# Performance work log

Hardware: AMD Instinct MI355X
Metric: run time of the kernel (lower is better)

## Reference

```python
import jax, jax.numpy as jnp
import numpy as np

N = 100000      # nodes
E = 1600000     # edges
F_IN = 64       # num_node_features
R = 8           # num_relations
G = 256         # graphs in batch
H, C = 4, 32    # GAT heads, per-head channels
NEG_SLOPE_ATT = 0.2    # GATConv attention leaky relu
NEG_SLOPE = 0.01       # F.leaky_relu default


def setup_inputs() -> dict:
    key = jax.random.key(0)
    ks = jax.random.split(key, 12)
    init = lambda k, shape, fan: (jax.random.normal(k, shape, jnp.float32) / np.sqrt(fan).astype(np.float32))
    x = jax.random.normal(ks[0], (N, F_IN), jnp.float32)
    edge_index = jax.random.randint(ks[1], (2, E), 0, N)
    edge_type = jax.random.randint(ks[2], (E,), 0, R)
    batch = (jnp.arange(N) * G) // N  # sorted graph ids, every segment non-empty
    return dict(
        x=x, edge_index=edge_index, edge_type=edge_type, batch=batch,
        gat_w=init(ks[3], (F_IN, H * C), F_IN),
        gat_att_src=init(ks[4], (H, C), C),
        gat_att_dst=init(ks[5], (H, C), C),
        gat_bias=jnp.zeros((H * C,), jnp.float32),
        dense1_w=init(ks[6], (H * C, 16), H * C),
        dense1_b=jnp.zeros((16,), jnp.float32),
        rw1=init(ks[7], (R, F_IN, 32), F_IN),
        root1=init(ks[8], (F_IN, 32), F_IN),
        rb1=jnp.zeros((32,), jnp.float32),
        rw2=init(ks[9], (R, 32, 16), 32),
        root2=init(ks[10], (32, 16), 32),
        rb2=jnp.zeros((16,), jnp.float32),
        dense_w=init(ks[11], (32, 1), 32),
        dense_b=jnp.zeros((1,), jnp.float32),
    )


def _gat(x, src, dst, w, att_src, att_dst, bias):
    h = (x @ w).reshape(N, H, C)                       # [N,H,C]
    a_src = jnp.sum(h * att_src, axis=-1)              # [N,H]
    a_dst = jnp.sum(h * att_dst, axis=-1)              # [N,H]
    e = jax.nn.leaky_relu(a_src[src] + a_dst[dst], NEG_SLOPE_ATT)  # [E,H]
    # segment softmax over incoming edges of each dst node
    m = jax.ops.segment_max(e, dst, num_segments=N)    # [N,H]
    p = jnp.exp(e - m[dst])
    s = jax.ops.segment_sum(p, dst, num_segments=N)    # [N,H]
    alpha = p / s[dst]
    msg = h[src] * alpha[:, :, None]                   # [E,H,C]
    out = jax.ops.segment_sum(msg, dst, num_segments=N)
    return out.reshape(N, H * C) + bias


def _rgcn(x, src, dst, edge_type, w, root, bias):
    # per-relation transform of all nodes, then edge gather (PyG RGCNConv, aggr='mean')
    xw = jnp.einsum('ni,rio->rno', x, w)               # [R,N,out]
    msg = xw[edge_type, src]                           # [E,out]
    comb = dst * R + edge_type                         # mean is per (dst, relation)
    cnt = jax.ops.segment_sum(jnp.ones((E,), x.dtype), comb, num_segments=N * R)
    agg = jax.ops.segment_sum(msg / cnt[comb][:, None], dst, num_segments=N)
    return agg + x @ root + bias


def reference(x, edge_index, edge_type, batch, gat_w, gat_att_src, gat_att_dst,
              gat_bias, dense1_w, dense1_b, rw1, root1, rb1, rw2, root2, rb2,
              dense_w, dense_b):
    src, dst = edge_index[0], edge_index[1]
    # GAT branch (dropout treated as identity / eval mode)
    h = _gat(x, src, dst, gat_w, gat_att_src, gat_att_dst, gat_bias)
    h = jax.nn.leaky_relu(h, NEG_SLOPE)
    h = jax.nn.leaky_relu(h @ dense1_w + dense1_b, NEG_SLOPE)
    gmax = jax.ops.segment_max(h, batch, num_segments=G)          # [G,16]
    # RGCN branch
    z = jax.nn.relu(_rgcn(x, src, dst, edge_type, rw1, root1, rb1))
    z = jax.nn.relu(_rgcn(z, src, dst, edge_type, rw2, root2, rb2))
    nodes_per_graph = jax.ops.segment_sum(jnp.ones((N,), x.dtype), batch, num_segments=G)
    gmean = jax.ops.segment_sum(z, batch, num_segments=G) / nodes_per_graph[:, None]
    # fuse
    zc = jnp.concatenate([gmax, gmean], axis=1)                   # [G,32]
    return zc @ dense_w + dense_b                                  # [G,1]
```

## Files before the change

kernel.cpp:

```cpp
#include <hip/hip_runtime.h>
#include <hip/hip_bf16.h>

typedef __hip_bfloat16 bf16;
typedef unsigned short u16;

#define N_NODES 100000
#define N_EDGES 1600000
#define F_IN 64
#define N_REL 8
#define N_GRAPH 256
#define N_HEAD 4
#define HC 128
#define NBLK_SCAN 391

__device__ __forceinline__ float lrelu(float x, float s) { return x >= 0.f ? x : s * x; }
__device__ __forceinline__ unsigned fenc(float f) {
  unsigned b = __float_as_uint(f);
  return (b & 0x80000000u) ? ~b : (b | 0x80000000u);
}
__device__ __forceinline__ float fdec(unsigned u) {
  float v = __uint_as_float((u & 0x80000000u) ? (u & 0x7fffffffu) : ~u);
  return fmaxf(fminf(v, 3e38f), -3e38f);
}
__device__ __forceinline__ float lo_bf(unsigned u) { return __uint_as_float(u << 16); }
__device__ __forceinline__ float hi_bf(unsigned u) { return __uint_as_float(u & 0xFFFF0000u); }
__device__ __forceinline__ bf16 f2bf(float v) { return __float2bfloat16(v); }
__device__ __forceinline__ unsigned f2bfu(float v) {
  unsigned u = __float_as_uint(v);
  return (u + 0x7FFFu + ((u >> 16) & 1u)) >> 16;
}

template<bool BF> __device__ __forceinline__ float ldf(const void* p, size_t i) {
  if (BF) { u16 v = ((const u16*)p)[i]; return __uint_as_float(((unsigned)v) << 16); }
  else    { return ((const float*)p)[i]; }
}
template<bool BF> __device__ __forceinline__ float2 ldf2(const void* p, size_t i) {
  if (BF) { unsigned v = ((const unsigned*)p)[i]; return make_float2(lo_bf(v), hi_bf(v)); }
  else    { return ((const float2*)p)[i]; }
}

__global__ void k_probe(const u16* __restrict__ xr, int* __restrict__ flag) {
  int t = threadIdx.x;
  int c = 0;
  for (int i = t; i < 1024; i += 256) {
    unsigned e = (xr[i] >> 7) & 0xFFu;
    if (e >= 100u && e <= 140u) c++;
  }
  __shared__ int sc[256];
  sc[t] = c;
  __syncthreads();
  for (int s = 128; s; s >>= 1) { if (t < s) sc[t] += sc[t + s]; __syncthreads(); }
  if (t == 0) *flag = (sc[0] >= 800) ? 1 : 0;
}

template<bool BF>
__device__ __forceinline__ void gat_h_body(const void* x, const void* w, const void* att_s,
                                           const void* att_d, u16* __restrict__ h,
                                           float* __restrict__ a_src, float* __restrict__ a_dst,
                                           int n, float* xs) {
  int j = threadIdx.x;
  if (j < F_IN) xs[j] = ldf<BF>(x, (size_t)n * F_IN + j);
  __syncthreads();
  float acc = 0.f;
#pragma unroll
  for (int k = 0; k < F_IN; ++k) acc += xs[k] * ldf<BF>(w, (size_t)k * HC + j);
  h[(size_t)n * HC + j] = (u16)f2bfu(acc);
  float ps = acc * ldf<BF>(att_s, j);
  float pd = acc * ldf<BF>(att_d, j);
#pragma unroll
  for (int off = 16; off > 0; off >>= 1) {
    ps += __shfl_down(ps, off, 32);
    pd += __shfl_down(pd, off, 32);
  }
  if ((j & 31) == 0) {
    a_src[n * N_HEAD + (j >> 5)] = ps;
    a_dst[n * N_HEAD + (j >> 5)] = pd;
  }
}

__global__ void k_gath_hist(const void* x, const void* w, const void* att_s, const void* att_d,
                            u16* h, float* a_src, float* a_dst,
                            const int* __restrict__ ei, const int* __restrict__ etype,
                            int* __restrict__ deg, int* __restrict__ cnt, const int* flag) {
  __shared__ float xs[F_IN];
  if (blockIdx.x < N_NODES) {
    if (__builtin_amdgcn_readfirstlane(*flag))
      gat_h_body<true>(x, w, att_s, att_d, h, a_src, a_dst, blockIdx.x, xs);
    else
      gat_h_body<false>(x, w, att_s, att_d, h, a_src, a_dst, blockIdx.x, xs);
  } else {
    int e = (blockIdx.x - N_NODES) * 128 + threadIdx.x;
    if (e < N_EDGES) {
      int d = ei[N_EDGES + e], t = etype[e];
      atomicAdd(&deg[d], 1);
      atomicAdd(&cnt[d * N_REL + t], 1);
    }
  }
}

__global__ void k_scan_a(const int* __restrict__ deg, int* __restrict__ rowptr,
                         int* __restrict__ scanblk) {
  __shared__ int buf[256];
  int tid = threadIdx.x;
  int i = blockIdx.x * 256 + tid;
  int v = (i < N_NODES) ? deg[i] : 0;
  buf[tid] = v;
  __syncthreads();
  for (int st = 1; st < 256; st <<= 1) {
    int t = buf[tid];
    int a = (tid >= st) ? buf[tid - st] : 0;
    __syncthreads();
    buf[tid] = t + a;
    __syncthreads();
  }
  if (i < N_NODES) rowptr[i] = buf[tid] - v;
  if (tid == 255) scanblk[blockIdx.x] = buf[255];
}
__global__ void k_scan_b(int* __restrict__ scanblk) {
  __shared__ int buf[512];
  int tid = threadIdx.x;
  int v = (tid < NBLK_SCAN) ? scanblk[tid] : 0;
  buf[tid] = v;
  __syncthreads();
  for (int st = 1; st < 512; st <<= 1) {
    int t = buf[tid];
    int a = (tid >= st) ? buf[tid - st] : 0;
    __syncthreads();
    buf[tid] = t + a;
    __syncthreads();
  }
  if (tid < NBLK_SCAN) scanblk[tid] = buf[tid] - v;
}
__global__ void k_scan_c(int* __restrict__ rowptr, int* __restrict__ wp,
                         const int* __restrict__ scanblk) {
  int i = blockIdx.x * 256 + threadIdx.x;
  if (i < N_NODES) {
    int val = rowptr[i] + scanblk[blockIdx.x];
    rowptr[i] = val;
    wp[i] = val;
  } else if (i == N_NODES) {
    rowptr[N_NODES] = N_EDGES;
  }
}

__global__ void k_scatter(const int* __restrict__ ei, const int* __restrict__ etype,
                          const float* __restrict__ a_src, const float* __restrict__ a_dst,
                          int* __restrict__ wp, unsigned* __restrict__ csr,
                          float4* __restrict__ p_logit) {
  int e = blockIdx.x * 256 + threadIdx.x;
  if (e >= N_EDGES) return;
  int sn = ei[e], d = ei[N_EDGES + e], t = etype[e];
  int pos = atomicAdd(&wp[d], 1);
  csr[pos] = (unsigned)sn | ((unsigned)t << 20);
  const float4 as = *(const float4*)&a_src[sn * 4];
  const float4 ad = *(const float4*)&a_dst[d * 4];
  float4 lg;
  lg.x = lrelu(as.x + ad.x, 0.2f);
  lg.y = lrelu(as.y + ad.y, 0.2f);
  lg.z = lrelu(as.z + ad.z, 0.2f);
  lg.w = lrelu(as.w + ad.w, 0.2f);
  p_logit[pos] = lg;
}

__global__ void k_msum(const int* __restrict__ rowptr, const float* __restrict__ p_logit,
                       float* __restrict__ m_arr, float* __restrict__ si_arr) {
  int tid = threadIdx.x;
  int n = blockIdx.x * 16 + (tid >> 4);
  int l16 = tid & 15, head = l16 & 3, slot = l16 >> 2;
  int base = rowptr[n], deg = rowptr[n + 1] - base;
  float m = -1e30f;
  for (int i = slot; i < deg; i += 4) m = fmaxf(m, p_logit[(size_t)(base + i) * 4 + head]);
  m = fmaxf(m, __shfl_xor(m, 4, 64));
  m = fmaxf(m, __shfl_xor(m, 8, 64));
  float s = 0.f;
  for (int i = slot; i < deg; i += 4) s += __expf(p_logit[(size_t)(base + i) * 4 + head] - m);
  s += __shfl_xor(s, 4, 64);
  s += __shfl_xor(s, 8, 64);
  if (slot == 0) {
    m_arr[n * 4 + head] = m;
    si_arr[n * 4 + head] = (deg > 0) ? 1.f / s : 0.f;
  }
}

template<bool BF>
__device__ __forceinline__ void gat_agg_body(const int* __restrict__ rowptr,
                                             const unsigned* __restrict__ csr,
                                             const float* __restrict__ lg,
                                             const float* __restrict__ m_arr,
                                             const float* __restrict__ si_arr,
                                             const uint2* __restrict__ hu2, const void* gbias,
                                             const void* d1w, const void* d1b,
                                             const int* __restrict__ batch,
                                             unsigned* __restrict__ gmax, int* __restrict__ npg,
                                             float (*os)[132]) {
  int tid = threadIdx.x;
  int wave = tid >> 6, l = tid & 63;
  int d = blockIdx.x * 4 + wave;
  int base = rowptr[d];
  int deg = rowptr[d + 1] - base;
  int slot = l >> 5, cl = l & 31;
  int head = cl >> 3;
  float m = m_arr[d * 4 + head];
  float si = si_arr[d * 4 + head];
  float a0 = 0.f, a1 = 0.f, a2 = 0.f, a3 = 0.f;
  int i = slot;
  for (; i + 6 < deg; i += 8) {
    unsigned sp0 = csr[base + i],     sp1 = csr[base + i + 2];
    unsigned sp2 = csr[base + i + 4], sp3 = csr[base + i + 6];
    float av0 = __expf(lg[(size_t)(base + i) * 4 + head] - m) * si;
    float av1 = __expf(lg[(size_t)(base + i + 2) * 4 + head] - m) * si;
    float av2 = __expf(lg[(size_t)(base + i + 4) * 4 + head] - m) * si;
    float av3 = __expf(lg[(size_t)(base + i + 6) * 4 + head] - m) * si;
    uint2 h0 = hu2[(size_t)(sp0 & 0xFFFFF) * 32 + cl];
    uint2 h1 = hu2[(size_t)(sp1 & 0xFFFFF) * 32 + cl];
    uint2 h2 = hu2[(size_t)(sp2 & 0xFFFFF) * 32 + cl];
    uint2 h3 = hu2[(size_t)(sp3 & 0xFFFFF) * 32 + cl];
    a0 += lo_bf(h0.x) * av0 + lo_bf(h1.x) * av1 + lo_bf(h2.x) * av2 + lo_bf(h3.x) * av3;
    a1 += hi_bf(h0.x) * av0 + hi_bf(h1.x) * av1 + hi_bf(h2.x) * av2 + hi_bf(h3.x) * av3;
    a2 += lo_bf(h0.y) * av0 + lo_bf(h1.y) * av1 + lo_bf(h2.y) * av2 + lo_bf(h3.y) * av3;
    a3 += hi_bf(h0.y) * av0 + hi_bf(h1.y) * av1 + hi_bf(h2.y) * av2 + hi_bf(h3.y) * av3;
  }
  for (; i < deg; i += 2) {
    unsigned sp = csr[base + i];
    float av = __expf(lg[(size_t)(base + i) * 4 + head] - m) * si;
    uint2 hv = hu2[(size_t)(sp & 0xFFFFF) * 32 + cl];
    a0 += lo_bf(hv.x) * av;
    a1 += hi_bf(hv.x) * av;
    a2 += lo_bf(hv.y) * av;
    a3 += hi_bf(hv.y) * av;
  }
  a0 += __shfl_xor(a0, 32, 64);
  a1 += __shfl_xor(a1, 32, 64);
  a2 += __shfl_xor(a2, 32, 64);
  a3 += __shfl_xor(a3, 32, 64);
  if (slot == 0) {
    os[wave][4 * cl + 0] = lrelu(a0 + ldf<BF>(gbias, 4 * cl + 0), 0.01f);
    os[wave][4 * cl + 1] = lrelu(a1 + ldf<BF>(gbias, 4 * cl + 1), 0.01f);
    os[wave][4 * cl + 2] = lrelu(a2 + ldf<BF>(gbias, 4 * cl + 2), 0.01f);
    os[wave][4 * cl + 3] = lrelu(a3 + ldf<BF>(gbias, 4 * cl + 3), 0.01f);
  }
  __syncthreads();
  if (tid < 64) {
    int node = tid >> 4, out = tid & 15;
    float acc = ldf<BF>(d1b, out);
#pragma unroll
    for (int k = 0; k < HC; ++k) acc += os[node][k] * ldf<BF>(d1w, (size_t)k * 16 + out);
    acc = lrelu(acc, 0.01f);
    atomicMax(&gmax[batch[blockIdx.x * 4 + node] * 16 + out], fenc(acc));
  }
  if (tid < 4) atomicAdd(&npg[batch[blockIdx.x * 4 + tid]], 1);
}
__global__ void k_gat_agg(const int* rowptr, const unsigned* csr, const float* lg,
                          const float* m_arr, const float* si_arr,
                          const u16* h, const void* gbias, const void* d1w, const void* d1b,
                          const int* batch, unsigned* gmax, int* npg, const int* flag) {
  __shared__ float os[4][132];
  if (__builtin_amdgcn_readfirstlane(*flag))
    gat_agg_body<true>(rowptr, csr, lg, m_arr, si_arr, (const uint2*)h, gbias, d1w, d1b,
                       batch, gmax, npg, os);
  else
    gat_agg_body<false>(rowptr, csr, lg, m_arr, si_arr, (const uint2*)h, gbias, d1w, d1b,
                        batch, gmax, npg, os);
}

template<bool BF>
__device__ __forceinline__ void xw1_body(const void* x, const void* rw1, bf16* __restrict__ xw1,
                                         int n0, int r, float (*xs)[F_IN]) {
  int tid = threadIdx.x;
  for (int i = tid; i < 8 * F_IN; i += 256) {
    int nn = n0 + (i >> 6);
    xs[i >> 6][i & 63] = (nn < N_NODES) ? ldf<BF>(x, (size_t)nn * F_IN + (i & 63)) : 0.f;
  }
  __syncthreads();
  int nl = tid >> 5, c = tid & 31;
  int n = n0 + nl;
  float acc = 0.f;
#pragma unroll
  for (int k = 0; k < F_IN; ++k) acc += xs[nl][k] * ldf<BF>(rw1, (size_t)(r * F_IN + k) * 32 + c);
  if (n < N_NODES) xw1[((size_t)r * N_NODES + n) * 32 + c] = f2bf(acc);
}
__global__ void k_xw1(const void* x, const void* rw1, bf16* xw1, const int* flag) {
  __shared__ float xs[8][F_IN];
  int n0 = blockIdx.x * 8, r = blockIdx.y;
  if (__builtin_amdgcn_readfirstlane(*flag)) xw1_body<true>(x, rw1, xw1, n0, r, xs);
  else xw1_body<false>(x, rw1, xw1, n0, r, xs);
}

template<bool BF>
__device__ __forceinline__ void ragg1_body(const int* __restrict__ rowptr,
                                           const unsigned* __restrict__ csr,
                                           const int* __restrict__ cnt,
                                           const unsigned* __restrict__ xw, const void* x,
                                           const void* root1, const void* rb1,
                                           float* __restrict__ z1,
                                           float (*xs)[F_IN], float (*cinv)[N_REL]) {
  int tid = threadIdx.x;
  int n0 = blockIdx.x * 4;
  {
    int nn = n0 + (tid >> 6);
    xs[tid >> 6][tid & 63] = ldf<BF>(x, (size_t)nn * F_IN + (tid & 63));
  }
  if (tid < 32) {
    int cv = cnt[(n0 + (tid >> 3)) * N_REL + (tid & 7)];
    cinv[tid >> 3][tid & 7] = (cv > 0) ? 1.f / (float)cv : 0.f;
  }
  __syncthreads();
  int wave = tid >> 6, l = tid & 63;
  int slot = l >> 4, cl = l & 15;
  int n = n0 + wave;
  int base = rowptr[n], deg = rowptr[n + 1] - base;
  float a0 = 0.f, a1 = 0.f;
  int i = slot;
  for (; i + 4 < deg; i += 8) {
    unsigned sp0 = csr[base + i], sp1 = csr[base + i + 4];
    int t0 = sp0 >> 20, t1 = sp1 >> 20;
    unsigned v0 = xw[((size_t)t0 * N_NODES + (sp0 & 0xFFFFF)) * 16 + cl];
    unsigned v1 = xw[((size_t)t1 * N_NODES + (sp1 & 0xFFFFF)) * 16 + cl];
    float c0 = cinv[wave][t0], c1 = cinv[wave][t1];
    a0 += lo_bf(v0) * c0 + lo_bf(v1) * c1;
    a1 += hi_bf(v0) * c0 + hi_bf(v1) * c1;
  }
  if (i < deg) {
    unsigned sp = csr[base + i];
    int t = sp >> 20;
    unsigned v = xw[((size_t)t * N_NODES + (sp & 0xFFFFF)) * 16 + cl];
    float c0 = cinv[wave][t];
    a0 += lo_bf(v) * c0;
    a1 += hi_bf(v) * c0;
  }
#pragma unroll
  for (int kk = 0; kk < 16; ++kk) {
    int k = slot * 16 + kk;
    float xv = xs[wave][k];
    float2 wv = ldf2<BF>(root1, (size_t)k * 16 + cl);
    a0 += xv * wv.x;
    a1 += xv * wv.y;
  }
  a0 += __shfl_xor(a0, 16, 64); a0 += __shfl_xor(a0, 32, 64);
  a1 += __shfl_xor(a1, 16, 64); a1 += __shfl_xor(a1, 32, 64);
  if (slot == 0) {
    z1[(size_t)n * 32 + 2 * cl]     = fmaxf(a0 + ldf<BF>(rb1, 2 * cl), 0.f);
    z1[(size_t)n * 32 + 2 * cl + 1] = fmaxf(a1 + ldf<BF>(rb1, 2 * cl + 1), 0.f);
  }
}
__global__ void k_ragg1(const int* rowptr, const unsigned* csr, const int* cnt,
                        const bf16* xw1, const void* x, const void* root1, const void* rb1,
                        float* z1, const int* flag) {
  __shared__ float xs[4][F_IN];
  __shared__ float cinv[4][N_REL];
  if (__builtin_amdgcn_readfirstlane(*flag))
    ragg1_body<true>(rowptr, csr, cnt, (const unsigned*)xw1, x, root1, rb1, z1, xs, cinv);
  else
    ragg1_body<false>(rowptr, csr, cnt, (const unsigned*)xw1, x, root1, rb1, z1, xs, cinv);
}

template<bool BF>
__device__ __forceinline__ void zw2_body(const float* __restrict__ z1, const void* rw2,
                                         bf16* __restrict__ zw2, float (*zs)[32]) {
  int tid = threadIdx.x;
  int n0 = blockIdx.x * 16;
  for (int i = tid; i < 16 * 32; i += 256) {
    int nn = n0 + (i >> 5);
    zs[i >> 5][i & 31] = (nn < N_NODES) ? z1[(size_t)nn * 32 + (i & 31)] : 0.f;
  }
  __syncthreads();
  int nl = tid >> 4, c = tid & 15;
  int n = n0 + nl, r = blockIdx.y;
  float acc = 0.f;
#pragma unroll
  for (int k = 0; k < 32; ++k) acc += zs[nl][k] * ldf<BF>(rw2, (size_t)(r * 32 + k) * 16 + c);
  if (n < N_NODES) zw2[((size_t)r * N_NODES + n) * 16 + c] = f2bf(acc);
}
__global__ void k_zw2(const float* z1, const void* rw2, bf16* zw2, const int* flag) {
  __shared__ float zs[16][32];
  if (__builtin_amdgcn_readfirstlane(*flag)) zw2_body<true>(z1, rw2, zw2, zs);
  else zw2_body<false>(z1, rw2, zw2, zs);
}

template<bool BF>
__device__ __forceinline__ void ragg2_body(const int* __restrict__ rowptr,
                                           const unsigned* __restrict__ csr,
                                           const int* __restrict__ cnt,
                                           const unsigned* __restrict__ zw,
                                           const float* __restrict__ z1, const void* root2,
                                           const void* rb2, const int* __restrict__ batch,
                                           float* __restrict__ gsum,
                                           float (*zs)[33], float (*cinv)[N_REL]) {
  int tid = threadIdx.x;
  int n0 = blockIdx.x * 4;
  if (tid < 128) {
    int nn = n0 + (tid >> 5);
    zs[tid >> 5][tid & 31] = z1[(size_t)nn * 32 + (tid & 31)];
  }
  if (tid < 32) {
    int cv = cnt[(n0 + (tid >> 3)) * N_REL + (tid & 7)];
    cinv[tid >> 3][tid & 7] = (cv > 0) ? 1.f / (float)cv : 0.f;
  }
  __syncthreads();
  int wave = tid >> 6, l = tid & 63;
  int slot = l >> 3, cl = l & 7;
  int n = n0 + wave;
  int base = rowptr[n], deg = rowptr[n + 1] - base;
  float a0 = 0.f, a1 = 0.f;
  int i = slot;
  for (; i + 8 < deg; i += 16) {
    unsigned sp0 = csr[base + i], sp1 = csr[base + i + 8];
    int t0 = sp0 >> 20, t1 = sp1 >> 20;
    unsigned v0 = zw[((size_t)t0 * N_NODES + (sp0 & 0xFFFFF)) * 8 + cl];
    unsigned v1 = zw[((size_t)t1 * N_NODES + (sp1 & 0xFFFFF)) * 8 + cl];
    float c0 = cinv[wave][t0], c1 = cinv[wave][t1];
    a0 += lo_bf(v0) * c0 + lo_bf(v1) * c1;
    a1 += hi_bf(v0) * c0 + hi_bf(v1) * c1;
  }
  if (i < deg) {
    unsigned sp = csr[base + i];
    int t = sp >> 20;
    unsigned v = zw[((size_t)t * N_NODES + (sp & 0xFFFFF)) * 8 + cl];
    float c0 = cinv[wave][t];
    a0 += lo_bf(v) * c0;
    a1 += hi_bf(v) * c0;
  }
#pragma unroll
  for (int kk = 0; kk < 4; ++kk) {
    int k = slot * 4 + kk;
    float zv = zs[wave][k];
    float2 wv = ldf2<BF>(root2, (size_t)k * 8 + cl);
    a0 += zv * wv.x;
    a1 += zv * wv.y;
  }
  a0 += __shfl_xor(a0, 8, 64); a0 += __shfl_xor(a0, 16, 64); a0 += __shfl_xor(a0, 32, 64);
  a1 += __shfl_xor(a1, 8, 64); a1 += __shfl_xor(a1, 16, 64); a1 += __shfl_xor(a1, 32, 64);
  if (slot == 0) {
    float z2a = fmaxf(a0 + ldf<BF>(rb2, 2 * cl), 0.f);
    float z2b = fmaxf(a1 + ldf<BF>(rb2, 2 * cl + 1), 0.f);
    int g = batch[n];
    atomicAdd(&gsum[g * 16 + 2 * cl], z2a);
    atomicAdd(&gsum[g * 16 + 2 * cl + 1], z2b);
  }
}
__global__ void k_ragg2(const int* rowptr, const unsigned* csr, const int* cnt,
                        const bf16* zw2, const float* z1, const void* root2, const void* rb2,
                        const int* batch, float* gsum, const int* flag) {
  __shared__ float zs[4][33];
  __shared__ float cinv[4][N_REL];
  if (__builtin_amdgcn_readfirstlane(*flag))
    ragg2_body<true>(rowptr, csr, cnt, (const unsigned*)zw2, z1, root2, rb2, batch, gsum,
                     zs, cinv);
  else
    ragg2_body<false>(rowptr, csr, cnt, (const unsigned*)zw2, z1, root2, rb2, batch, gsum,
                      zs, cinv);
}

template<bool BF>
__device__ __forceinline__ void final_body(const unsigned* __restrict__ gmax,
                                           const float* __restrict__ gsum,
                                           const int* __restrict__ npg, const void* dw,
                                           const void* db, void* out) {
  int g = threadIdx.x;
  if (g >= N_GRAPH) return;
  float acc = ldf<BF>(db, 0);
  int np = npg[g]; if (np < 1) np = 1;
  float inv = 1.f / (float)np;
#pragma unroll
  for (int c = 0; c < 16; ++c) {
    acc += fdec(gmax[g * 16 + c]) * ldf<BF>(dw, c);
    acc += (gsum[g * 16 + c] * inv) * ldf<BF>(dw, 16 + c);
  }
  if (BF) ((bf16*)out)[g] = f2bf(acc);
  else ((float*)out)[g] = acc;
}
__global__ void k_final(const unsigned* gmax, const float* gsum, const int* npg,
                        const void* dw, const void* db, void* out, const int* flag) {
  if (__builtin_amdgcn_readfirstlane(*flag)) final_body<true>(gmax, gsum, npg, dw, db, out);
  else final_body<false>(gmax, gsum, npg, dw, db, out);
}

extern "C" void kernel_launch(void* const* d_in, const int* in_sizes, int n_in,
                              void* d_out, int out_size, void* d_ws, size_t ws_size,
                              hipStream_t stream) {
  const void* x        = d_in[0];
  const int*  ei       = (const int*)d_in[1];
  const int*  etype    = (const int*)d_in[2];
  const int*  batch    = (const int*)d_in[3];
  const void* gat_w    = d_in[4];
  const void* att_src  = d_in[5];
  const void* att_dst  = d_in[6];
  const void* gat_bias = d_in[7];
  const void* d1w      = d_in[8];
  const void* d1b      = d_in[9];
  const void* rw1      = d_in[10];
  const void* root1    = d_in[11];
  const void* rb1      = d_in[12];
  const void* rw2      = d_in[13];
  const void* root2    = d_in[14];
  const void* rb2      = d_in[15];
  const void* dw       = d_in[16];
  const void* db       = d_in[17];

  char* ws = (char*)d_ws;
  const size_t o_h     = 0;
  const size_t o_plog  = 25600000;
  const size_t o_xw1   = 51200000;
  const size_t o_zw2   = 0;
  const size_t o_asrc  = 102400000;
  const size_t o_adst  = 104000000;
  const size_t o_deg   = 105600000;
  const size_t o_rowp  = 106000000;
  const size_t o_wp    = 106400016;
  const size_t o_cnt   = 106800016;
  const size_t o_csr   = 110000016;
  const size_t o_z1    = 116400016;
  const size_t o_sblk  = 129200016;
  const size_t o_gmax  = 129201600;
  const size_t o_gsum  = 129217984;
  const size_t o_npg   = 129234368;
  const size_t o_flag  = 129235392;
  const size_t total   = 129235396;
  if (ws_size < total) return;

  u16*      h      = (u16*)(ws + o_h);
  float*    plog   = (float*)(ws + o_plog);
  bf16*     xw1    = (bf16*)(ws + o_xw1);
  bf16*     zw2    = (bf16*)(ws + o_zw2);
  float*    a_src  = (float*)(ws + o_asrc);
  float*    a_dst  = (float*)(ws + o_adst);
  int*      deg    = (int*)(ws + o_deg);
  int*      rowptr = (int*)(ws + o_rowp);
  int*      wp     = (int*)(ws + o_wp);
  int*      cnt    = (int*)(ws + o_cnt);
  unsigned* csr    = (unsigned*)(ws + o_csr);
  float*    z1     = (float*)(ws + o_z1);
  int*      sblk   = (int*)(ws + o_sblk);
  unsigned* gmax   = (unsigned*)(ws + o_gmax);
  float*    gsum   = (float*)(ws + o_gsum);
  int*      npg    = (int*)(ws + o_npg);
  int*      flag   = (int*)(ws + o_flag);

  k_probe<<<1, 256, 0, stream>>>((const u16*)x, flag);

  hipMemsetAsync(ws + o_deg, 0, o_csr - o_deg, stream);
  hipMemsetAsync(ws + o_gmax, 0, 33792, stream);

  k_gath_hist<<<N_NODES + 12500, 128, 0, stream>>>(x, gat_w, att_src, att_dst, h,
                                                   a_src, a_dst, ei, etype, deg, cnt, flag);

  k_scan_a<<<NBLK_SCAN, 256, 0, stream>>>(deg, rowptr, sblk);
  k_scan_b<<<1, 512, 0, stream>>>(sblk);
  k_scan_c<<<NBLK_SCAN, 256, 0, stream>>>(rowptr, wp, sblk);
  k_scatter<<<(N_EDGES + 255) / 256, 256, 0, stream>>>(ei, etype, a_src, a_dst, wp, csr,
                                                       (float4*)plog);

  k_msum<<<N_NODES / 16, 256, 0, stream>>>(rowptr, plog, a_src, a_dst);

  k_gat_agg<<<N_NODES / 4, 256, 0, stream>>>(rowptr, csr, plog, a_src, a_dst, h, gat_bias,
                                             d1w, d1b, batch, gmax, npg, flag);

  k_xw1<<<dim3((N_NODES + 7) / 8, N_REL), 256, 0, stream>>>(x, rw1, xw1, flag);
  k_ragg1<<<N_NODES / 4, 256, 0, stream>>>(rowptr, csr, cnt, xw1, x, root1, rb1, z1, flag);

  k_zw2<<<dim3((N_NODES + 15) / 16, N_REL), 256, 0, stream>>>(z1, rw2, zw2, flag);
  k_ragg2<<<N_NODES / 4, 256, 0, stream>>>(rowptr, csr, cnt, zw2, z1, root2, rb2,
                                           batch, gsum, flag);

  k_final<<<1, 256, 0, stream>>>(gmax, gsum, npg, dw, db, d_out, flag);
}
```

Before: 1.268 ms.

## Recompute GAT edge logits on the fly and fuse zw2 transform into ragg1

The scatter kernel no longer writes a per-edge float4 logit buffer. The softmax-stats and aggregation kernels instead recompute each logit from a gathered a_src value and the node's a_dst, which removes a large edge-sized write and its three later reads. Separately, the layer-2 per-relation transform (z1 @ rw2) is computed inside ragg1 right after z1 is produced, which drops the separate k_zw2 launch and its re-read of z1. In exchange there are more random gathers into the small a_src array, extra exp/lrelu math, and more work and a second barrier inside ragg1.

```diff
diff --git a/kernel.cpp b/kernel.cpp
--- a/kernel.cpp
+++ b/kernel.cpp
@@ -144,36 +144,34 @@
 }
 
 __global__ void k_scatter(const int* __restrict__ ei, const int* __restrict__ etype,
-                          const float* __restrict__ a_src, const float* __restrict__ a_dst,
-                          int* __restrict__ wp, unsigned* __restrict__ csr,
-                          float4* __restrict__ p_logit) {
+                          int* __restrict__ wp, unsigned* __restrict__ csr) {
   int e = blockIdx.x * 256 + threadIdx.x;
   if (e >= N_EDGES) return;
   int sn = ei[e], d = ei[N_EDGES + e], t = etype[e];
   int pos = atomicAdd(&wp[d], 1);
   csr[pos] = (unsigned)sn | ((unsigned)t << 20);
-  const float4 as = *(const float4*)&a_src[sn * 4];
-  const float4 ad = *(const float4*)&a_dst[d * 4];
-  float4 lg;
-  lg.x = lrelu(as.x + ad.x, 0.2f);
-  lg.y = lrelu(as.y + ad.y, 0.2f);
-  lg.z = lrelu(as.z + ad.z, 0.2f);
-  lg.w = lrelu(as.w + ad.w, 0.2f);
-  p_logit[pos] = lg;
-}
-
-__global__ void k_msum(const int* __restrict__ rowptr, const float* __restrict__ p_logit,
+}
+
+__global__ void k_msum(const int* __restrict__ rowptr, const unsigned* __restrict__ csr,
+                       const float* __restrict__ a_src, const float* __restrict__ a_dst,
                        float* __restrict__ m_arr, float* __restrict__ si_arr) {
   int tid = threadIdx.x;
   int n = blockIdx.x * 16 + (tid >> 4);
   int l16 = tid & 15, head = l16 & 3, slot = l16 >> 2;
   int base = rowptr[n], deg = rowptr[n + 1] - base;
+  float ad = a_dst[n * 4 + head];
   float m = -1e30f;
-  for (int i = slot; i < deg; i += 4) m = fmaxf(m, p_logit[(size_t)(base + i) * 4 + head]);
+  for (int i = slot; i < deg; i += 4) {
+    unsigned sp = csr[base + i];
+    m = fmaxf(m, lrelu(a_src[(sp & 0xFFFFF) * 4 + head] + ad, 0.2f));
+  }
   m = fmaxf(m, __shfl_xor(m, 4, 64));
   m = fmaxf(m, __shfl_xor(m, 8, 64));
   float s = 0.f;
-  for (int i = slot; i < deg; i += 4) s += __expf(p_logit[(size_t)(base + i) * 4 + head] - m);
+  for (int i = slot; i < deg; i += 4) {
+    unsigned sp = csr[base + i];
+    s += __expf(lrelu(a_src[(sp & 0xFFFFF) * 4 + head] + ad, 0.2f) - m);
+  }
   s += __shfl_xor(s, 4, 64);
   s += __shfl_xor(s, 8, 64);
   if (slot == 0) {
@@ -185,7 +183,8 @@
 template<bool BF>
 __device__ __forceinline__ void gat_agg_body(const int* __restrict__ rowptr,
                                              const unsigned* __restrict__ csr,
-                                             const float* __restrict__ lg,
+                                             const float* __restrict__ asrc,
+                                             const float* __restrict__ adst,
                                              const float* __restrict__ m_arr,
                                              const float* __restrict__ si_arr,
                                              const uint2* __restrict__ hu2, const void* gbias,
@@ -202,19 +201,24 @@
   int head = cl >> 3;
   float m = m_arr[d * 4 + head];
   float si = si_arr[d * 4 + head];
+  float adv = adst[d * 4 + head];
   float a0 = 0.f, a1 = 0.f, a2 = 0.f, a3 = 0.f;
   int i = slot;
   for (; i + 6 < deg; i += 8) {
     unsigned sp0 = csr[base + i],     sp1 = csr[base + i + 2];
     unsigned sp2 = csr[base + i + 4], sp3 = csr[base + i + 6];
-    float av0 = __expf(lg[(size_t)(base + i) * 4 + head] - m) * si;
-    float av1 = __expf(lg[(size_t)(base + i + 2) * 4 + head] - m) * si;
-    float av2 = __expf(lg[(size_t)(base + i + 4) * 4 + head] - m) * si;
-    float av3 = __expf(lg[(size_t)(base + i + 6) * 4 + head] - m) * si;
+    float as0 = asrc[(sp0 & 0xFFFFF) * 4 + head];
+    float as1 = asrc[(sp1 & 0xFFFFF) * 4 + head];
+    float as2 = asrc[(sp2 & 0xFFFFF) * 4 + head];
+    float as3 = asrc[(sp3 & 0xFFFFF) * 4 + head];
     uint2 h0 = hu2[(size_t)(sp0 & 0xFFFFF) * 32 + cl];
     uint2 h1 = hu2[(size_t)(sp1 & 0xFFFFF) * 32 + cl];
     uint2 h2 = hu2[(size_t)(sp2 & 0xFFFFF) * 32 + cl];
     uint2 h3 = hu2[(size_t)(sp3 & 0xFFFFF) * 32 + cl];
+    float av0 = __expf(lrelu(as0 + adv, 0.2f) - m) * si;
+    float av1 = __expf(lrelu(as1 + adv, 0.2f) - m) * si;
+    float av2 = __expf(lrelu(as2 + adv, 0.2f) - m) * si;
+    float av3 = __expf(lrelu(as3 + adv, 0.2f) - m) * si;
     a0 += lo_bf(h0.x) * av0 + lo_bf(h1.x) * av1 + lo_bf(h2.x) * av2 + lo_bf(h3.x) * av3;
     a1 += hi_bf(h0.x) * av0 + hi_bf(h1.x) * av1 + hi_bf(h2.x) * av2 + hi_bf(h3.x) * av3;
     a2 += lo_bf(h0.y) * av0 + lo_bf(h1.y) * av1 + lo_bf(h2.y) * av2 + lo_bf(h3.y) * av3;
@@ -222,7 +226,7 @@
   }
   for (; i < deg; i += 2) {
     unsigned sp = csr[base + i];
-    float av = __expf(lg[(size_t)(base + i) * 4 + head] - m) * si;
+    float av = __expf(lrelu(asrc[(sp & 0xFFFFF) * 4 + head] + adv, 0.2f) - m) * si;
     uint2 hv = hu2[(size_t)(sp & 0xFFFFF) * 32 + cl];
     a0 += lo_bf(hv.x) * av;
     a1 += hi_bf(hv.x) * av;
@@ -250,17 +254,17 @@
   }
   if (tid < 4) atomicAdd(&npg[batch[blockIdx.x * 4 + tid]], 1);
 }
-__global__ void k_gat_agg(const int* rowptr, const unsigned* csr, const float* lg,
-                          const float* m_arr, const float* si_arr,
+__global__ void k_gat_agg(const int* rowptr, const unsigned* csr, const float* asrc,
+                          const float* adst, const float* m_arr, const float* si_arr,
                           const u16* h, const void* gbias, const void* d1w, const void* d1b,
                           const int* batch, unsigned* gmax, int* npg, const int* flag) {
   __shared__ float os[4][132];
   if (__builtin_amdgcn_readfirstlane(*flag))
-    gat_agg_body<true>(rowptr, csr, lg, m_arr, si_arr, (const uint2*)h, gbias, d1w, d1b,
-                       batch, gmax, npg, os);
+    gat_agg_body<true>(rowptr, csr, asrc, adst, m_arr, si_arr, (const uint2*)h, gbias,
+                       d1w, d1b, batch, gmax, npg, os);
   else
-    gat_agg_body<false>(rowptr, csr, lg, m_arr, si_arr, (const uint2*)h, gbias, d1w, d1b,
-                        batch, gmax, npg, os);
+    gat_agg_body<false>(rowptr, csr, asrc, adst, m_arr, si_arr, (const uint2*)h, gbias,
+                        d1w, d1b, batch, gmax, npg, os);
 }
 
 template<bool BF>
@@ -292,8 +296,10 @@
                                            const int* __restrict__ cnt,
                                            const unsigned* __restrict__ xw, const void* x,
                                            const void* root1, const void* rb1,
-                                           float* __restrict__ z1,
-                                           float (*xs)[F_IN], float (*cinv)[N_REL]) {
+                                           const void* rw2,
+                                           float* __restrict__ z1, unsigned* __restrict__ zw2u,
+                                           float (*xs)[F_IN], float (*cinv)[N_REL],
+                                           float (*zsl)[32]) {
   int tid = threadIdx.x;
   int n0 = blockIdx.x * 4;
   {
@@ -339,42 +345,41 @@
   a0 += __shfl_xor(a0, 16, 64); a0 += __shfl_xor(a0, 32, 64);
   a1 += __shfl_xor(a1, 16, 64); a1 += __shfl_xor(a1, 32, 64);
   if (slot == 0) {
-    z1[(size_t)n * 32 + 2 * cl]     = fmaxf(a0 + ldf<BF>(rb1, 2 * cl), 0.f);
-    z1[(size_t)n * 32 + 2 * cl + 1] = fmaxf(a1 + ldf<BF>(rb1, 2 * cl + 1), 0.f);
+    float z0 = fmaxf(a0 + ldf<BF>(rb1, 2 * cl), 0.f);
+    float z1v = fmaxf(a1 + ldf<BF>(rb1, 2 * cl + 1), 0.f);
+    z1[(size_t)n * 32 + 2 * cl]     = z0;
+    z1[(size_t)n * 32 + 2 * cl + 1] = z1v;
+    zsl[wave][2 * cl]     = z0;
+    zsl[wave][2 * cl + 1] = z1v;
+  }
+  __syncthreads();
+  {
+    int node = tid >> 6, idx = tid & 63;
+    int r = idx >> 3, c8 = idx & 7;
+    float s0 = 0.f, s1 = 0.f;
+#pragma unroll
+    for (int k = 0; k < 32; ++k) {
+      float zv = zsl[node][k];
+      float2 wv = ldf2<BF>(rw2, (size_t)(r * 32 + k) * 8 + c8);
+      s0 += zv * wv.x;
+      s1 += zv * wv.y;
+    }
+    int nn = n0 + node;
+    zw2u[((size_t)r * N_NODES + nn) * 8 + c8] = (f2bfu(s1) << 16) | f2bfu(s0);
   }
 }
 __global__ void k_ragg1(const int* rowptr, const unsigned* csr, const int* cnt,
                         const bf16* xw1, const void* x, const void* root1, const void* rb1,
-                        float* z1, const int* flag) {
+                        const void* rw2, float* z1, bf16* zw2, const int* flag) {
   __shared__ float xs[4][F_IN];
   __shared__ float cinv[4][N_REL];
+  __shared__ float zsl[4][32];
   if (__builtin_amdgcn_readfirstlane(*flag))
-    ragg1_body<true>(rowptr, csr, cnt, (const unsigned*)xw1, x, root1, rb1, z1, xs, cinv);
+    ragg1_body<true>(rowptr, csr, cnt, (const unsigned*)xw1, x, root1, rb1, rw2, z1,
+                     (unsigned*)zw2, xs, cinv, zsl);
   else
-    ragg1_body<false>(rowptr, csr, cnt, (const unsigned*)xw1, x, root1, rb1, z1, xs, cinv);
-}
-
-template<bool BF>
-__device__ __forceinline__ void zw2_body(const float* __restrict__ z1, const void* rw2,
-                                         bf16* __restrict__ zw2, float (*zs)[32]) {
-  int tid = threadIdx.x;
-  int n0 = blockIdx.x * 16;
-  for (int i = tid; i < 16 * 32; i += 256) {
-    int nn = n0 + (i >> 5);
-    zs[i >> 5][i & 31] = (nn < N_NODES) ? z1[(size_t)nn * 32 + (i & 31)] : 0.f;
-  }
-  __syncthreads();
-  int nl = tid >> 4, c = tid & 15;
-  int n = n0 + nl, r = blockIdx.y;
-  float acc = 0.f;
-#pragma unroll
-  for (int k = 0; k < 32; ++k) acc += zs[nl][k] * ldf<BF>(rw2, (size_t)(r * 32 + k) * 16 + c);
-  if (n < N_NODES) zw2[((size_t)r * N_NODES + n) * 16 + c] = f2bf(acc);
-}
-__global__ void k_zw2(const float* z1, const void* rw2, bf16* zw2, const int* flag) {
-  __shared__ float zs[16][32];
-  if (__builtin_amdgcn_readfirstlane(*flag)) zw2_body<true>(z1, rw2, zw2, zs);
-  else zw2_body<false>(z1, rw2, zw2, zs);
+    ragg1_body<false>(rowptr, csr, cnt, (const unsigned*)xw1, x, root1, rb1, rw2, z1,
+                      (unsigned*)zw2, xs, cinv, zsl);
 }
 
 template<bool BF>
@@ -499,31 +504,33 @@
 
   char* ws = (char*)d_ws;
   const size_t o_h     = 0;
-  const size_t o_plog  = 25600000;
-  const size_t o_xw1   = 51200000;
+  const size_t o_xw1   = 25600000;
   const size_t o_zw2   = 0;
-  const size_t o_asrc  = 102400000;
-  const size_t o_adst  = 104000000;
-  const size_t o_deg   = 105600000;
-  const size_t o_rowp  = 106000000;
-  const size_t o_wp    = 106400016;
-  const size_t o_cnt   = 106800016;
-  const size_t o_csr   = 110000016;
-  const size_t o_z1    = 116400016;
-  const size_t o_sblk  = 129200016;
-  const size_t o_gmax  = 129201600;
-  const size_t o_gsum  = 129217984;
-  const size_t o_npg   = 129234368;
-  const size_t o_flag  = 129235392;
-  const size_t total   = 129235396;
+  const size_t o_asrc  = 76800000;
+  const size_t o_adst  = 78400000;
+  const size_t o_m     = 80000000;
+  const size_t o_si    = 81600000;
+  const size_t o_deg   = 83200000;
+  const size_t o_rowp  = 83600000;
+  const size_t o_wp    = 84000016;
+  const size_t o_cnt   = 84400032;
+  const size_t o_csr   = 87600032;
+  const size_t o_z1    = 94000032;
+  const size_t o_sblk  = 106800032;
+  const size_t o_gmax  = 106801600;
+  const size_t o_gsum  = 106817984;
+  const size_t o_npg   = 106834368;
+  const size_t o_flag  = 106835392;
+  const size_t total   = 106835396;
   if (ws_size < total) return;
 
   u16*      h      = (u16*)(ws + o_h);
-  float*    plog   = (float*)(ws + o_plog);
   bf16*     xw1    = (bf16*)(ws + o_xw1);
   bf16*     zw2    = (bf16*)(ws + o_zw2);
   float*    a_src  = (float*)(ws + o_asrc);
   float*    a_dst  = (float*)(ws + o_adst);
+  float*    m_arr  = (float*)(ws + o_m);
+  float*    si_arr = (float*)(ws + o_si);
   int*      deg    = (int*)(ws + o_deg);
   int*      rowptr = (int*)(ws + o_rowp);
   int*      wp     = (int*)(ws + o_wp);
@@ -547,18 +554,17 @@
   k_scan_a<<<NBLK_SCAN, 256, 0, stream>>>(deg, rowptr, sblk);
   k_scan_b<<<1, 512, 0, stream>>>(sblk);
   k_scan_c<<<NBLK_SCAN, 256, 0, stream>>>(rowptr, wp, sblk);
-  k_scatter<<<(N_EDGES + 255) / 256, 256, 0, stream>>>(ei, etype, a_src, a_dst, wp, csr,
-                                                       (float4*)plog);
-
-  k_msum<<<N_NODES / 16, 256, 0, stream>>>(rowptr, plog, a_src, a_dst);
-
-  k_gat_agg<<<N_NODES / 4, 256, 0, stream>>>(rowptr, csr, plog, a_src, a_dst, h, gat_bias,
-                                             d1w, d1b, batch, gmax, npg, flag);
+  k_scatter<<<(N_EDGES + 255) / 256, 256, 0, stream>>>(ei, etype, wp, csr);
+
+  k_msum<<<N_NODES / 16, 256, 0, stream>>>(rowptr, csr, a_src, a_dst, m_arr, si_arr);
+
+  k_gat_agg<<<N_NODES / 4, 256, 0, stream>>>(rowptr, csr, a_src, a_dst, m_arr, si_arr, h,
+                                             gat_bias, d1w, d1b, batch, gmax, npg, flag);
 
   k_xw1<<<dim3((N_NODES + 7) / 8, N_REL), 256, 0, stream>>>(x, rw1, xw1, flag);
-  k_ragg1<<<N_NODES / 4, 256, 0, stream>>>(rowptr, csr, cnt, xw1, x, root1, rb1, z1, flag);
-
-  k_zw2<<<dim3((N_NODES + 15) / 16, N_REL), 256, 0, stream>>>(z1, rw2, zw2, flag);
+  k_ragg1<<<N_NODES / 4, 256, 0, stream>>>(rowptr, csr, cnt, xw1, x, root1, rb1, rw2,
+                                           z1, zw2, flag);
+
   k_ragg2<<<N_NODES / 4, 256, 0, stream>>>(rowptr, csr, cnt, zw2, z1, root2, rb2,
                                            batch, gsum, flag);
 
```

Measured after the change: 1.403 ms. 1.11x slower.
